# Kernel optimization log

Hardware: AMD Instinct MI355X
Metric: run time of the kernel (lower is better)

Reference implementation:

```python
import jax, jax.numpy as jnp
import numpy as np

NUM_BLOCKS = 6
D_MODEL = 1024
D_FF = 4096
NUM_HEADS = 16
NIN = 32
SEQ = NIN + 1  # +1 for SOS/EOS slot in the order-respecting mask
BATCH = 1024
D_HEAD = D_MODEL // NUM_HEADS
NEG = 1e10


def _order_masks(n):
    # order_respecting_mask with natural ordering arange(n)
    m0 = np.zeros((n + 1, n + 1), np.int32)  # input-layer mask
    m0[:, 0] = 1
    for s in range(n):
        for d in range(s + 1, n):
            m0[d, s + 1] = 1
    m0[-1, :] = 0
    mr = np.zeros((n + 1, n + 1), np.int32)  # later-layer mask (sees self)
    for s in range(n):
        for d in range(s, n):
            mr[d, s] = 1
    return jnp.asarray(m0), jnp.asarray(mr)


def setup_inputs() -> dict:
    key = jax.random.key(0)
    ks = jax.random.split(key, 6)
    std = 0.02  # Conv1d init std
    L, D, F = NUM_BLOCKS, D_MODEL, D_FF
    m0, mr = _order_masks(NIN)
    return {
        "x": jax.random.normal(ks[0], (BATCH, SEQ, D), jnp.float32),
        "qkv_w": std * jax.random.normal(ks[1], (L, D, 3 * D), jnp.float32),
        "qkv_b": jnp.zeros((L, 3 * D), jnp.float32),
        "proj_w": std * jax.random.normal(ks[2], (L, D, D), jnp.float32),
        "proj_b": jnp.zeros((L, D), jnp.float32),
        "w1": std * jax.random.normal(ks[3], (L, D, F), jnp.float32),
        "b1": jnp.zeros((L, F), jnp.float32),
        "w2": std * jax.random.normal(ks[4], (L, F, D), jnp.float32),
        "b2": jnp.zeros((L, D), jnp.float32),
        "ln1_s": jnp.ones((L, D), jnp.float32),
        "ln1_b": jnp.zeros((L, D), jnp.float32),
        "ln2_s": jnp.ones((L, D), jnp.float32),
        "ln2_b": jnp.zeros((L, D), jnp.float32),
        "lnf_s": jnp.ones((D,), jnp.float32),
        "lnf_b": jnp.zeros((D,), jnp.float32),
        "mask0": m0,
        "mask_rest": mr,
    }


def _ln(h, scale, shift, eps=1e-5):
    mean = h.mean(-1, keepdims=True)
    var = jnp.mean((h - mean) ** 2, axis=-1, keepdims=True)
    return scale * ((h - mean) * jax.lax.rsqrt(var + eps)) + shift


def _forward(x, qkv_w, qkv_b, proj_w, proj_b, w1, b1, w2, b2,
             ln1_s, ln1_b, ln2_s, ln2_b, lnf_s, lnf_b, mask0, mask_rest):
    B, S, D = x.shape
    H, Dh = NUM_HEADS, D_HEAD
    inv_sqrt_dk = 1.0 / np.sqrt(Dh).astype(np.float32)
    for l in range(qkv_w.shape[0]):
        m = (mask0 if l == 0 else mask_rest).astype(x.dtype)  # [S,S]
        h = _ln(x, ln1_s[l], ln1_b[l])
        qkv = h @ qkv_w[l] + qkv_b[l]  # [B,S,3D]
        q, k, v = [t.reshape(B, S, H, Dh) for t in jnp.split(qkv, 3, axis=-1)]
        scores = jnp.einsum('bshd,bthd->bhst', q, k) * inv_sqrt_dk  # [B,H,S,S]
        scores = scores * m - (1.0 - m) * NEG  # multiplicative+additive mask, as in source
        attn = jax.nn.softmax(scores, axis=-1)
        o = jnp.einsum('bhst,bthd->bshd', attn, v).reshape(B, S, D)
        x = x + (o @ proj_w[l] + proj_b[l])  # residual
        h = _ln(x, ln2_s[l], ln2_b[l])
        x = x + (jax.nn.gelu(h @ w1[l] + b1[l], approximate=False) @ w2[l] + b2[l])
    return _ln(x, lnf_s, lnf_b)  # ln_output=True


def reference(x, qkv_w, qkv_b, proj_w, proj_b, w1, b1, w2, b2,
              ln1_s, ln1_b, ln2_s, ln2_b, lnf_s, lnf_b, mask0, mask_rest):
    return _forward(x, qkv_w, qkv_b, proj_w, proj_b, w1, b1, w2, b2,
                    ln1_s, ln1_b, ln2_s, ln2_b, lnf_s, lnf_b, mask0, mask_rest)
```

## Files before the change

kernel.cpp:

```cpp
#include <hip/hip_runtime.h>

typedef unsigned short u16;
typedef __attribute__((ext_vector_type(8))) short s16x8;
typedef __attribute__((ext_vector_type(4))) float f32x4;

__device__ __forceinline__ float b2f(u16 u){ union{unsigned int i; float f;} v; v.i=((unsigned int)u)<<16; return v.f; }
__device__ __forceinline__ u16 f2b(float f){ union{float f; unsigned int i;} v; v.f=f; unsigned int r=v.i+0x7FFFu+((v.i>>16)&1u); return (u16)(r>>16); }

__device__ __forceinline__ void gload16(const void* g, void* l){
  __builtin_amdgcn_global_load_lds((const __attribute__((address_space(1))) void*)g,
                                   (__attribute__((address_space(3))) void*)l, 16, 0, 0);
}

__global__ void probe_k(const unsigned int* __restrict__ w, int* __restrict__ flag){
  if (threadIdx.x==0 && blockIdx.x==0) flag[0] = (w[0]!=0x3F800000u) ? 1 : 0;
}

__global__ __launch_bounds__(256) void conv2f32_k(const void* __restrict__ src, float* __restrict__ dst,
                                                  int n, const int* __restrict__ flag){
  const bool isb = flag[0]!=0;
  int i = (blockIdx.x*256+threadIdx.x)*4;
  for (int e=0;e<4;e++){
    int j=i+e;
    if (j<n) dst[j] = isb ? b2f(((const u16*)src)[j]) : ((const float*)src)[j];
  }
}

__global__ __launch_bounds__(256) void conv2bf16_k(const void* __restrict__ src, u16* __restrict__ dst,
                                                   int n, const int* __restrict__ flag){
  const bool isb = flag[0]!=0;
  int i = (blockIdx.x*256+threadIdx.x)*4;
  for (int e=0;e<4;e++){
    int j=i+e;
    if (j<n) dst[j] = isb ? ((const u16*)src)[j] : f2b(((const float*)src)[j]);
  }
}

__global__ __launch_bounds__(256) void transconv_k(const void* __restrict__ W, size_t ebase,
                                                   u16* __restrict__ Wt, int K, int Nc,
                                                   const int* __restrict__ flag){
  __shared__ float t[32][33];
  const bool isb = flag[0]!=0;
  const int n0 = blockIdx.x*32, k0 = blockIdx.y*32;
  const int tx = threadIdx.x, ty = threadIdx.y;
  #pragma unroll
  for (int r=0;r<4;r++){
    int row = ty + r*8;
    size_t idx = ebase + (size_t)(k0+row)*Nc + n0 + tx;
    t[row][tx] = isb ? b2f(((const u16*)W)[idx]) : ((const float*)W)[idx];
  }
  __syncthreads();
  #pragma unroll
  for (int r=0;r<4;r++){
    int row = ty + r*8;
    Wt[(size_t)(n0+row)*K + k0 + tx] = f2b(t[tx][row]);
  }
}

template<int XF32>
__global__ __launch_bounds__(256) void ln_k(const void* __restrict__ Xv, const float* __restrict__ sc,
                                            const float* __restrict__ sh, u16* __restrict__ O){
  const size_t t = blockIdx.x;
  const int tid = threadIdx.x;
  float x0,x1,x2,x3;
  if (XF32){
    float4 f = ((const float4*)Xv)[t*256 + tid];
    x0=f.x; x1=f.y; x2=f.z; x3=f.w;
  } else {
    uint2 u = *(const uint2*)((const u16*)Xv + t*1024 + tid*4);
    x0=b2f((u16)(u.x&0xFFFF)); x1=b2f((u16)(u.x>>16)); x2=b2f((u16)(u.y&0xFFFF)); x3=b2f((u16)(u.y>>16));
  }
  float s = x0+x1+x2+x3;
  float q = x0*x0+x1*x1+x2*x2+x3*x3;
  #pragma unroll
  for (int off=32; off; off>>=1){ s += __shfl_xor(s, off, 64); q += __shfl_xor(q, off, 64); }
  __shared__ float as[4], aq[4];
  if ((tid&63)==0){ as[tid>>6]=s; aq[tid>>6]=q; }
  __syncthreads();
  s = as[0]+as[1]+as[2]+as[3];
  q = aq[0]+aq[1]+aq[2]+aq[3];
  float mean = s*(1.0f/1024.0f);
  float var  = q*(1.0f/1024.0f) - mean*mean;
  float rs = rsqrtf(var + 1e-5f);
  int c = tid*4;
  float y0 = sc[c+0]*((x0-mean)*rs)+sh[c+0];
  float y1 = sc[c+1]*((x1-mean)*rs)+sh[c+1];
  float y2 = sc[c+2]*((x2-mean)*rs)+sh[c+2];
  float y3 = sc[c+3]*((x3-mean)*rs)+sh[c+3];
  uint2 o; o.x=(unsigned)f2b(y0)|((unsigned)f2b(y1)<<16); o.y=(unsigned)f2b(y2)|((unsigned)f2b(y3)<<16);
  *(uint2*)(O + t*1024 + tid*4) = o;
}

template<int XF32>
__global__ __launch_bounds__(256) void ln_out_k(const void* __restrict__ Xv, const float* __restrict__ sc,
                                                const float* __restrict__ sh, void* __restrict__ out,
                                                const int* __restrict__ flag){
  const size_t t = blockIdx.x;
  const int tid = threadIdx.x;
  float x0,x1,x2,x3;
  if (XF32){
    float4 f = ((const float4*)Xv)[t*256 + tid];
    x0=f.x; x1=f.y; x2=f.z; x3=f.w;
  } else {
    uint2 u = *(const uint2*)((const u16*)Xv + t*1024 + tid*4);
    x0=b2f((u16)(u.x&0xFFFF)); x1=b2f((u16)(u.x>>16)); x2=b2f((u16)(u.y&0xFFFF)); x3=b2f((u16)(u.y>>16));
  }
  float s = x0+x1+x2+x3;
  float q = x0*x0+x1*x1+x2*x2+x3*x3;
  #pragma unroll
  for (int off=32; off; off>>=1){ s += __shfl_xor(s, off, 64); q += __shfl_xor(q, off, 64); }
  __shared__ float as[4], aq[4];
  if ((tid&63)==0){ as[tid>>6]=s; aq[tid>>6]=q; }
  __syncthreads();
  s = as[0]+as[1]+as[2]+as[3];
  q = aq[0]+aq[1]+aq[2]+aq[3];
  float mean = s*(1.0f/1024.0f);
  float var  = q*(1.0f/1024.0f) - mean*mean;
  float rs = rsqrtf(var + 1e-5f);
  int c = tid*4;
  float y0 = sc[c+0]*((x0-mean)*rs)+sh[c+0];
  float y1 = sc[c+1]*((x1-mean)*rs)+sh[c+1];
  float y2 = sc[c+2]*((x2-mean)*rs)+sh[c+2];
  float y3 = sc[c+3]*((x3-mean)*rs)+sh[c+3];
  if (flag[0]){
    uint2 o; o.x=(unsigned)f2b(y0)|((unsigned)f2b(y1)<<16); o.y=(unsigned)f2b(y2)|((unsigned)f2b(y3)<<16);
    *(uint2*)((u16*)out + t*1024 + tid*4) = o;
  } else {
    float4 o4; o4.x=y0; o4.y=y1; o4.z=y2; o4.w=y3;
    ((float4*)out)[t*256 + tid] = o4;
  }
}

__global__ __launch_bounds__(128) void attn_k(const u16* __restrict__ QKV, const int* __restrict__ mask,
                                              u16* __restrict__ O){
  __shared__ float q[33][65];
  __shared__ float ks[33][65];
  __shared__ float vs[33][65];
  __shared__ float p[33][34];
  const int tid = threadIdx.x;
  const int b = blockIdx.x>>4, h = blockIdx.x&15;
  const size_t tok0 = (size_t)b*33;
  for (int idx=tid; idx<33*16; idx+=128){
    int s=idx>>4, d4=(idx&15)*4;
    size_t base=(tok0+s)*3072 + h*64 + d4;
    uint2 uq=*(const uint2*)(QKV+base);
    uint2 uk=*(const uint2*)(QKV+base+1024);
    uint2 uv=*(const uint2*)(QKV+base+2048);
    q[s][d4+0]=b2f((u16)(uq.x&0xFFFF)); q[s][d4+1]=b2f((u16)(uq.x>>16));
    q[s][d4+2]=b2f((u16)(uq.y&0xFFFF)); q[s][d4+3]=b2f((u16)(uq.y>>16));
    ks[s][d4+0]=b2f((u16)(uk.x&0xFFFF)); ks[s][d4+1]=b2f((u16)(uk.x>>16));
    ks[s][d4+2]=b2f((u16)(uk.y&0xFFFF)); ks[s][d4+3]=b2f((u16)(uk.y>>16));
    vs[s][d4+0]=b2f((u16)(uv.x&0xFFFF)); vs[s][d4+1]=b2f((u16)(uv.x>>16));
    vs[s][d4+2]=b2f((u16)(uv.y&0xFFFF)); vs[s][d4+3]=b2f((u16)(uv.y>>16));
  }
  __syncthreads();
  for (int idx=tid; idx<33*9; idx+=128){
    int s=idx/9, tg=idx-s*9;
    int t0=tg*4;
    float a0=0.f,a1=0.f,a2=0.f,a3=0.f;
    if (t0<=s && s<32){
      int t1=min(t0+1,32), t2=min(t0+2,32), t3=min(t0+3,32);
      #pragma unroll
      for (int d=0; d<64; d++){
        float qq=q[s][d];
        a0+=qq*ks[t0][d]; a1+=qq*ks[t1][d]; a2+=qq*ks[t2][d]; a3+=qq*ks[t3][d];
      }
    }
    float av[4]={a0,a1,a2,a3};
    #pragma unroll
    for (int e=0;e<4;e++){
      int t=t0+e;
      if (t<33) p[s][t] = mask[s*33+t] ? av[e]*0.125f : -1e10f;
    }
  }
  __syncthreads();
  if (tid<33){
    float mx=-3.4e38f;
    for (int t=0;t<33;t++) mx = fmaxf(mx, p[tid][t]);
    float sm=0.f;
    for (int t=0;t<33;t++){ float e=expf(p[tid][t]-mx); p[tid][t]=e; sm+=e; }
    float inv=1.0f/sm;
    for (int t=0;t<33;t++) p[tid][t]*=inv;
  }
  __syncthreads();
  for (int idx=tid; idx<33*16; idx+=128){
    int s=idx>>4, d4=(idx&15)*4;
    float a0=0.f,a1=0.f,a2=0.f,a3=0.f;
    for (int t=0;t<=s;t++){
      float pp=p[s][t];
      a0+=pp*vs[t][d4+0]; a1+=pp*vs[t][d4+1]; a2+=pp*vs[t][d4+2]; a3+=pp*vs[t][d4+3];
    }
    uint2 o; o.x=(unsigned)f2b(a0)|((unsigned)f2b(a1)<<16); o.y=(unsigned)f2b(a2)|((unsigned)f2b(a3)<<16);
    *(uint2*)(O + (tok0+s)*1024 + h*64 + d4) = o;
  }
}

template<int MODE>
__global__ __launch_bounds__(256) void gemm_k(const u16* __restrict__ A, const u16* __restrict__ Bt,
                                              const float* __restrict__ bias, void* __restrict__ Cv,
                                              int Nc, int K){
  __shared__ __align__(16) u16 As[128*64];
  __shared__ __align__(16) u16 Bs[128*64];
  const int tid = threadIdx.x;
  const int wave = tid>>6, lane = tid&63;
  const int m0 = blockIdx.y*128, n0 = blockIdx.x*128;
  const int wm = (wave>>1)*64, wn = (wave&1)*64;
  const int r15 = lane&15, kg = lane>>4;
  f32x4 acc[4][4];
  #pragma unroll
  for (int i=0;i<4;i++)
    #pragma unroll
    for (int j=0;j<4;j++) acc[i][j] = (f32x4){0.f,0.f,0.f,0.f};

  for (int k0=0;k0<K;k0+=64){
    __syncthreads();
    #pragma unroll
    for (int i=0;i<4;i++){
      int c = tid + i*256;
      int r = c>>3, cc = c&7;
      int gcc = cc ^ (r&7);
      gload16(A  + (size_t)(m0+r)*K + k0 + gcc*8, As + (size_t)(i*256+wave*64)*8);
      gload16(Bt + (size_t)(n0+r)*K + k0 + gcc*8, Bs + (size_t)(i*256+wave*64)*8);
    }
    __syncthreads();
    #pragma unroll
    for (int ks=0;ks<2;ks++){
      s16x8 a[4], b[4];
      const int crd = ((ks*4+kg) ^ (r15&7))*8;
      #pragma unroll
      for (int i=0;i<4;i++) a[i] = *(const s16x8*)(As + (size_t)(wm + i*16 + r15)*64 + crd);
      #pragma unroll
      for (int j=0;j<4;j++) b[j] = *(const s16x8*)(Bs + (size_t)(wn + j*16 + r15)*64 + crd);
      #pragma unroll
      for (int i=0;i<4;i++)
        #pragma unroll
        for (int j=0;j<4;j++)
          acc[i][j] = __builtin_amdgcn_mfma_f32_16x16x32_bf16(a[i], b[j], acc[i][j], 0, 0, 0);
    }
  }
  #pragma unroll
  for (int i=0;i<4;i++){
    #pragma unroll
    for (int j=0;j<4;j++){
      int col = n0 + wn + j*16 + r15;
      float bc = bias[col];
      #pragma unroll
      for (int r=0;r<4;r++){
        int row = m0 + wm + i*16 + kg*4 + r;
        float vv = acc[i][j][r] + bc;
        if (MODE==1) vv = 0.5f*vv*(1.0f + erff(vv*0.70710678118f));
        size_t idx = (size_t)row*Nc + col;
        if (MODE==2){
          float* C = (float*)Cv;
          C[idx] += vv;
        } else if (MODE==3){
          u16* C = (u16*)Cv;
          C[idx] = f2b(vv + b2f(C[idx]));
        } else {
          ((u16*)Cv)[idx] = f2b(vv);
        }
      }
    }
  }
}

extern "C" void kernel_launch(void* const* d_in, const int* in_sizes, int n_in,
                              void* d_out, int out_size, void* d_ws, size_t ws_size,
                              hipStream_t stream){
  (void)in_sizes; (void)n_in; (void)out_size;
  const int L=6, D=1024, TD=3072, F=4096, NTOK=1024*33;
  const size_t PARAMN = 81920;

  auto need = [&](int xf32, int mc)->size_t{
    size_t t=0;
    auto add=[&](size_t b){ t=(t+255)&~(size_t)255; t+=b; };
    add((size_t)NTOK*D*(xf32?4:2)); add(PARAMN*4); add(4);
    add((size_t)mc*D*2); add((size_t)mc*F*2);
    add((size_t)TD*D*2); add((size_t)D*D*2); add((size_t)F*D*2); add((size_t)D*F*2);
    return t;
  };
  int xf32 = 1, mc = 8448;
  if (ws_size < need(1,8448)){
    mc = 4224;
    if (ws_size < need(1,4224)) xf32 = 0;
  }
  const int nch = NTOK/mc;

  char* basep = (char*)d_ws; size_t off=0;
  auto alloc=[&](size_t b)->char*{ off=(off+255)&~(size_t)255; char* p=basep+off; off+=b; return p; };
  void*  X   = (void*)alloc((size_t)NTOK*D*(xf32?4:2));
  float* pf  = (float*)alloc(PARAMN*4);
  int*   flag= (int*)alloc(4);
  u16*   H   = (u16*)alloc((size_t)mc*D*2);
  u16*   BIG = (u16*)alloc((size_t)mc*F*2);
  u16*   wQ  = (u16*)alloc((size_t)TD*D*2);
  u16*   wP  = (u16*)alloc((size_t)D*D*2);
  u16*   w1  = (u16*)alloc((size_t)F*D*2);
  u16*   w2  = (u16*)alloc((size_t)D*F*2);

  const size_t pQB=0, pPB=pQB+(size_t)L*TD, pB1=pPB+(size_t)L*D, pB2=pB1+(size_t)L*F,
               pL1S=pB2+(size_t)L*D, pL1B=pL1S+(size_t)L*D, pL2S=pL1B+(size_t)L*D,
               pL2B=pL2S+(size_t)L*D, pLFS=pL2B+(size_t)L*D, pLFB=pLFS+D;

  probe_k<<<1,64,0,stream>>>((const unsigned int*)d_in[9], flag);
  if (xf32) conv2f32_k<<<(NTOK*D)/1024,256,0,stream>>>(d_in[0], (float*)X, NTOK*D, flag);
  else      conv2bf16_k<<<(NTOK*D)/1024,256,0,stream>>>(d_in[0], (u16*)X, NTOK*D, flag);
  {
    struct PRM { int idx; size_t offe; int n; };
    const PRM prm[10] = {
      {2,pQB,L*TD},{4,pPB,L*D},{6,pB1,L*F},{8,pB2,L*D},
      {9,pL1S,L*D},{10,pL1B,L*D},{11,pL2S,L*D},{12,pL2B,L*D},
      {13,pLFS,D},{14,pLFB,D}};
    for (int i=0;i<10;i++)
      conv2f32_k<<<(prm[i].n+1023)/1024,256,0,stream>>>(d_in[prm[i].idx], pf+prm[i].offe, prm[i].n, flag);
  }

  const size_t xstride = (size_t)D*(xf32?4:2);
  for (int l=0;l<L;l++){
    transconv_k<<<dim3(TD/32, D/32), dim3(32,8),0,stream>>>(d_in[1], (size_t)l*D*TD, wQ, D, TD, flag);
    transconv_k<<<dim3(D/32,  D/32), dim3(32,8),0,stream>>>(d_in[3], (size_t)l*D*D,  wP, D, D,  flag);
    transconv_k<<<dim3(F/32,  D/32), dim3(32,8),0,stream>>>(d_in[5], (size_t)l*D*F,  w1, D, F,  flag);
    transconv_k<<<dim3(D/32,  F/32), dim3(32,8),0,stream>>>(d_in[7], (size_t)l*F*D,  w2, F, D,  flag);
    const int* msk = (const int*)d_in[l==0?15:16];
    for (int c=0;c<nch;c++){
      void* Xc = (void*)((char*)X + (size_t)c*mc*xstride);
      if (xf32){
        ln_k<1><<<mc,256,0,stream>>>(Xc, pf+pL1S+(size_t)l*D, pf+pL1B+(size_t)l*D, H);
        gemm_k<0><<<dim3(TD/128, mc/128),256,0,stream>>>(H, wQ, pf+pQB+(size_t)l*TD, BIG, TD, D);
        attn_k<<<(mc/33)*16,128,0,stream>>>(BIG, msk, H);
        gemm_k<2><<<dim3(D/128, mc/128),256,0,stream>>>(H, wP, pf+pPB+(size_t)l*D, Xc, D, D);
        ln_k<1><<<mc,256,0,stream>>>(Xc, pf+pL2S+(size_t)l*D, pf+pL2B+(size_t)l*D, H);
        gemm_k<1><<<dim3(F/128, mc/128),256,0,stream>>>(H, w1, pf+pB1+(size_t)l*F, BIG, F, D);
        gemm_k<2><<<dim3(D/128, mc/128),256,0,stream>>>(BIG, w2, pf+pB2+(size_t)l*D, Xc, D, F);
      } else {
        ln_k<0><<<mc,256,0,stream>>>(Xc, pf+pL1S+(size_t)l*D, pf+pL1B+(size_t)l*D, H);
        gemm_k<0><<<dim3(TD/128, mc/128),256,0,stream>>>(H, wQ, pf+pQB+(size_t)l*TD, BIG, TD, D);
        attn_k<<<(mc/33)*16,128,0,stream>>>(BIG, msk, H);
        gemm_k<3><<<dim3(D/128, mc/128),256,0,stream>>>(H, wP, pf+pPB+(size_t)l*D, Xc, D, D);
        ln_k<0><<<mc,256,0,stream>>>(Xc, pf+pL2S+(size_t)l*D, pf+pL2B+(size_t)l*D, H);
        gemm_k<1><<<dim3(F/128, mc/128),256,0,stream>>>(H, w1, pf+pB1+(size_t)l*F, BIG, F, D);
        gemm_k<3><<<dim3(D/128, mc/128),256,0,stream>>>(BIG, w2, pf+pB2+(size_t)l*D, Xc, D, F);
      }
    }
  }
  if (xf32) ln_out_k<1><<<NTOK,256,0,stream>>>(X, pf+pLFS, pf+pLFB, d_out, flag);
  else      ln_out_k<0><<<NTOK,256,0,stream>>>(X, pf+pLFS, pf+pLFB, d_out, flag);
}
```

Measured before the change: 10.58 ms.

## Replace GEMM with double-buffered 512-thread kernel and XCD-aware tile remap

Replaces the 128x128 single-buffered GEMM with a 512-thread kernel using 256-wide N tiles and 128- or 256-row M tiles. Global-to-LDS loads are double-buffered with explicit vmcnt waits and barriers, MFMA sections run at raised wave priority, and block IDs are remapped so neighbouring tiles share an XCD. The goal is to hide load latency behind compute and improve L2 reuse. The workspace fallback now prefers a bf16 residual stream at full chunk size before halving the chunk, which can lower residual precision when workspace is tight. Much larger LDS use may reduce occupancy.

```diff
diff --git a/kernel.cpp b/kernel.cpp
--- a/kernel.cpp
+++ b/kernel.cpp
@@ -195,64 +195,114 @@
   }
 }
 
-template<int MODE>
-__global__ __launch_bounds__(256) void gemm_k(const u16* __restrict__ A, const u16* __restrict__ Bt,
-                                              const float* __restrict__ bias, void* __restrict__ Cv,
-                                              int Nc, int K){
-  __shared__ __align__(16) u16 As[128*64];
-  __shared__ __align__(16) u16 Bs[128*64];
+template<int BM_, int MODE>
+__global__ __launch_bounds__(512,2) void gemm2_k(const u16* __restrict__ A, const u16* __restrict__ Bt,
+                                                 const float* __restrict__ bias, void* __restrict__ Cv,
+                                                 int Nc, int K){
+  constexpr int WROWS = BM_/2;
+  constexpr int MREP  = WROWS/16;
+  constexpr int IPP   = MREP/4;
+  constexpr int ALOADS= BM_/64;
+  __shared__ u16 As[2][BM_*64];
+  __shared__ u16 Bs[2][256*64];
   const int tid = threadIdx.x;
-  const int wave = tid>>6, lane = tid&63;
-  const int m0 = blockIdx.y*128, n0 = blockIdx.x*128;
-  const int wm = (wave>>1)*64, wn = (wave&1)*64;
+  const int wid = tid>>6, lane = tid&63;
+  const int wmid = wid>>2, wnid = wid&3;
   const int r15 = lane&15, kg = lane>>4;
-  f32x4 acc[4][4];
-  #pragma unroll
-  for (int i=0;i<4;i++)
+
+  const int gx = gridDim.x;
+  int id = blockIdx.y*gx + blockIdx.x;
+  const int nwg = gx*gridDim.y;
+  const int q8 = nwg>>3, r8 = nwg&7;
+  const int xcd = id&7; id >>= 3;
+  const int nid = (xcd<r8 ? xcd*(q8+1) : r8*(q8+1)+(xcd-r8)*q8) + id;
+  const int m0 = (nid/gx)*BM_, n0 = (nid%gx)*256;
+
+  const int NT = K>>6;
+
+  f32x4 acc[MREP][4];
+  #pragma unroll
+  for (int i=0;i<MREP;i++)
     #pragma unroll
     for (int j=0;j<4;j++) acc[i][j] = (f32x4){0.f,0.f,0.f,0.f};
 
-  for (int k0=0;k0<K;k0+=64){
-    __syncthreads();
+  auto stage = [&](int kt, int buf){
+    #pragma unroll
+    for (int i=0;i<ALOADS;i++){
+      int c=i*512+tid, row=c>>3, gs=(c&7)^(row&7);
+      gload16(A + (size_t)(m0+row)*K + kt*64 + gs*8, &As[buf][(size_t)c*8]);
+    }
     #pragma unroll
     for (int i=0;i<4;i++){
-      int c = tid + i*256;
-      int r = c>>3, cc = c&7;
-      int gcc = cc ^ (r&7);
-      gload16(A  + (size_t)(m0+r)*K + k0 + gcc*8, As + (size_t)(i*256+wave*64)*8);
-      gload16(Bt + (size_t)(n0+r)*K + k0 + gcc*8, Bs + (size_t)(i*256+wave*64)*8);
-    }
-    __syncthreads();
-    #pragma unroll
-    for (int ks=0;ks<2;ks++){
-      s16x8 a[4], b[4];
-      const int crd = ((ks*4+kg) ^ (r15&7))*8;
+      int c=i*512+tid, row=c>>3, gs=(c&7)^(row&7);
+      gload16(Bt + (size_t)(n0+row)*K + kt*64 + gs*8, &Bs[buf][(size_t)c*8]);
+    }
+  };
+
+  stage(0,0);
+  if (NT>1) stage(1,1);
+  asm volatile("s_waitcnt vmcnt(0)" ::: "memory");
+  __builtin_amdgcn_s_barrier();
+
+  s16x8 bfr[4][2];
+  for (int kt=0; kt<NT; ++kt){
+    const int cur = kt&1;
+    #pragma unroll
+    for (int q=0;q<4;q++){
+      if (q==0){
+        #pragma unroll
+        for (int j=0;j<4;j++){
+          int cl = wnid*64 + j*16 + r15;
+          #pragma unroll
+          for (int ks=0;ks<2;ks++)
+            bfr[j][ks] = *(const s16x8*)&Bs[cur][(size_t)cl*64 + (((ks*4+kg)^(r15&7))<<3)];
+        }
+      }
+      s16x8 afr[IPP][2];
       #pragma unroll
-      for (int i=0;i<4;i++) a[i] = *(const s16x8*)(As + (size_t)(wm + i*16 + r15)*64 + crd);
+      for (int ii=0;ii<IPP;ii++){
+        int rl = wmid*WROWS + (q*IPP+ii)*16 + r15;
+        #pragma unroll
+        for (int ks=0;ks<2;ks++)
+          afr[ii][ks] = *(const s16x8*)&As[cur][(size_t)rl*64 + (((ks*4+kg)^(r15&7))<<3)];
+      }
+      __builtin_amdgcn_s_barrier();
+      __builtin_amdgcn_s_setprio(1);
       #pragma unroll
-      for (int j=0;j<4;j++) b[j] = *(const s16x8*)(Bs + (size_t)(wn + j*16 + r15)*64 + crd);
-      #pragma unroll
-      for (int i=0;i<4;i++)
+      for (int ii=0;ii<IPP;ii++)
         #pragma unroll
         for (int j=0;j<4;j++)
-          acc[i][j] = __builtin_amdgcn_mfma_f32_16x16x32_bf16(a[i], b[j], acc[i][j], 0, 0, 0);
-    }
-  }
-  #pragma unroll
-  for (int i=0;i<4;i++){
+          #pragma unroll
+          for (int ks=0;ks<2;ks++)
+            acc[q*IPP+ii][j] = __builtin_amdgcn_mfma_f32_16x16x32_bf16(afr[ii][ks], bfr[j][ks], acc[q*IPP+ii][j], 0, 0, 0);
+      __builtin_amdgcn_s_setprio(0);
+    }
+    if (kt==NT-1) break;
+    __builtin_amdgcn_s_barrier();
+    if (kt+2<NT){
+      stage(kt+2, cur);
+      if constexpr (BM_==256) asm volatile("s_waitcnt vmcnt(8)" ::: "memory");
+      else                    asm volatile("s_waitcnt vmcnt(6)" ::: "memory");
+    } else {
+      asm volatile("s_waitcnt vmcnt(0)" ::: "memory");
+    }
+    __builtin_amdgcn_s_barrier();
+  }
+
+  #pragma unroll
+  for (int i=0;i<MREP;i++){
     #pragma unroll
     for (int j=0;j<4;j++){
-      int col = n0 + wn + j*16 + r15;
+      int col = n0 + wnid*64 + j*16 + r15;
       float bc = bias[col];
       #pragma unroll
       for (int r=0;r<4;r++){
-        int row = m0 + wm + i*16 + kg*4 + r;
+        int row = m0 + wmid*WROWS + i*16 + kg*4 + r;
         float vv = acc[i][j][r] + bc;
         if (MODE==1) vv = 0.5f*vv*(1.0f + erff(vv*0.70710678118f));
         size_t idx = (size_t)row*Nc + col;
         if (MODE==2){
-          float* C = (float*)Cv;
-          C[idx] += vv;
+          ((float*)Cv)[idx] += vv;
         } else if (MODE==3){
           u16* C = (u16*)Cv;
           C[idx] = f2b(vv + b2f(C[idx]));
@@ -281,10 +331,11 @@
   };
   int xf32 = 1, mc = 8448;
   if (ws_size < need(1,8448)){
-    mc = 4224;
-    if (ws_size < need(1,4224)) xf32 = 0;
+    xf32 = 0;
+    if (ws_size < need(0,8448)) mc = 4224;
   }
   const int nch = NTOK/mc;
+  const int bm256 = (mc%256)==0;
 
   char* basep = (char*)d_ws; size_t off=0;
   auto alloc=[&](size_t b)->char*{ off=(off+255)&~(size_t)255; char* p=basep+off; off+=b; return p; };
@@ -324,23 +375,19 @@
     const int* msk = (const int*)d_in[l==0?15:16];
     for (int c=0;c<nch;c++){
       void* Xc = (void*)((char*)X + (size_t)c*mc*xstride);
-      if (xf32){
-        ln_k<1><<<mc,256,0,stream>>>(Xc, pf+pL1S+(size_t)l*D, pf+pL1B+(size_t)l*D, H);
-        gemm_k<0><<<dim3(TD/128, mc/128),256,0,stream>>>(H, wQ, pf+pQB+(size_t)l*TD, BIG, TD, D);
-        attn_k<<<(mc/33)*16,128,0,stream>>>(BIG, msk, H);
-        gemm_k<2><<<dim3(D/128, mc/128),256,0,stream>>>(H, wP, pf+pPB+(size_t)l*D, Xc, D, D);
-        ln_k<1><<<mc,256,0,stream>>>(Xc, pf+pL2S+(size_t)l*D, pf+pL2B+(size_t)l*D, H);
-        gemm_k<1><<<dim3(F/128, mc/128),256,0,stream>>>(H, w1, pf+pB1+(size_t)l*F, BIG, F, D);
-        gemm_k<2><<<dim3(D/128, mc/128),256,0,stream>>>(BIG, w2, pf+pB2+(size_t)l*D, Xc, D, F);
-      } else {
-        ln_k<0><<<mc,256,0,stream>>>(Xc, pf+pL1S+(size_t)l*D, pf+pL1B+(size_t)l*D, H);
-        gemm_k<0><<<dim3(TD/128, mc/128),256,0,stream>>>(H, wQ, pf+pQB+(size_t)l*TD, BIG, TD, D);
-        attn_k<<<(mc/33)*16,128,0,stream>>>(BIG, msk, H);
-        gemm_k<3><<<dim3(D/128, mc/128),256,0,stream>>>(H, wP, pf+pPB+(size_t)l*D, Xc, D, D);
-        ln_k<0><<<mc,256,0,stream>>>(Xc, pf+pL2S+(size_t)l*D, pf+pL2B+(size_t)l*D, H);
-        gemm_k<1><<<dim3(F/128, mc/128),256,0,stream>>>(H, w1, pf+pB1+(size_t)l*F, BIG, F, D);
-        gemm_k<3><<<dim3(D/128, mc/128),256,0,stream>>>(BIG, w2, pf+pB2+(size_t)l*D, Xc, D, F);
-      }
+      if (xf32) ln_k<1><<<mc,256,0,stream>>>(Xc, pf+pL1S+(size_t)l*D, pf+pL1B+(size_t)l*D, H);
+      else      ln_k<0><<<mc,256,0,stream>>>(Xc, pf+pL1S+(size_t)l*D, pf+pL1B+(size_t)l*D, H);
+      if (bm256) gemm2_k<256,0><<<dim3(TD/256, mc/256),512,0,stream>>>(H, wQ, pf+pQB+(size_t)l*TD, BIG, TD, D);
+      else       gemm2_k<128,0><<<dim3(TD/256, mc/128),512,0,stream>>>(H, wQ, pf+pQB+(size_t)l*TD, BIG, TD, D);
+      attn_k<<<(mc/33)*16,128,0,stream>>>(BIG, msk, H);
+      if (xf32) gemm2_k<128,2><<<dim3(D/256, mc/128),512,0,stream>>>(H, wP, pf+pPB+(size_t)l*D, Xc, D, D);
+      else      gemm2_k<128,3><<<dim3(D/256, mc/128),512,0,stream>>>(H, wP, pf+pPB+(size_t)l*D, Xc, D, D);
+      if (xf32) ln_k<1><<<mc,256,0,stream>>>(Xc, pf+pL2S+(size_t)l*D, pf+pL2B+(size_t)l*D, H);
+      else      ln_k<0><<<mc,256,0,stream>>>(Xc, pf+pL2S+(size_t)l*D, pf+pL2B+(size_t)l*D, H);
+      if (bm256) gemm2_k<256,1><<<dim3(F/256, mc/256),512,0,stream>>>(H, w1, pf+pB1+(size_t)l*F, BIG, F, D);
+      else       gemm2_k<128,1><<<dim3(F/256, mc/128),512,0,stream>>>(H, w1, pf+pB1+(size_t)l*F, BIG, F, D);
+      if (xf32) gemm2_k<128,2><<<dim3(D/256, mc/128),512,0,stream>>>(BIG, w2, pf+pB2+(size_t)l*D, Xc, D, F);
+      else      gemm2_k<128,3><<<dim3(D/256, mc/128),512,0,stream>>>(BIG, w2, pf+pB2+(size_t)l*D, Xc, D, F);
     }
   }
   if (xf32) ln_out_k<1><<<NTOK,256,0,stream>>>(X, pf+pLFS, pf+pLFB, d_out, flag);
```

Result: slower. 14.37 ms (+35.8%).
